# Performance work log

Measured on AMD Instinct MI355X. Metric: run time of the kernel, lower is better.

The kernel has to match this reference:

```python
import jax, jax.numpy as jnp
import numpy as np

V, D, F, B, E = 50257, 1024, 2048, 64, 512  # vocab, embed/rnn dim, fc hidden, batch, entities


def setup_inputs() -> dict:
    key = jax.random.key(0)
    ks = jax.random.split(key, 12)
    s = 0.05
    return {
        "entity_hiddens": jax.random.normal(ks[0], (B, E, D), jnp.float32),
        "question": jax.random.randint(ks[1], (B,), 0, V),
        "keys_mask": jax.random.randint(ks[2], (B, E), 0, 2).astype(bool),
        "emb": jax.random.normal(ks[3], (V, D), jnp.float32) * s,
        "W1": jax.random.normal(ks[4], (D, F), jnp.float32) * s,
        "b1": jnp.zeros((F,), jnp.float32),
        "W2": jax.random.normal(ks[5], (F, D), jnp.float32) * s,
        "b2": jnp.zeros((D,), jnp.float32),
        "A": jax.random.normal(ks[6], (D, D), jnp.float32) * s,  # entity_attn_matrix
        "H": jax.random.normal(ks[7], (D, D), jnp.float32) * s,
        "Ws": jax.random.normal(ks[8], (D, V), jnp.float32) * s,
        "bs": jnp.zeros((V,), jnp.float32),
    }


def reference(entity_hiddens, question, keys_mask, emb, W1, b1, W2, b2, A, H, Ws, bs):
    # embed question token and project: [B, D]
    eq0 = emb[question]
    q = jax.nn.relu(eq0 @ W1 + b1) @ W2 + b2
    # attention_entities actual returned math:
    # reduce_sum(expand_dims(q@A,1) * boolean_mask(entities, mask), axis=1)
    # == (q @ A) * sum over all masked entities (a single [D] vector)
    qA = q @ A  # [B, D]
    m = keys_mask.astype(entity_hiddens.dtype)
    ent_sum = jnp.sum(entity_hiddens * m[..., None], axis=(0, 1))  # [D]
    u = qA * ent_sum  # [B, D]
    logits = (q + u @ H) @ Ws + bs  # [B, V]
    return jax.nn.softmax(logits, axis=-1)
```

## Files before the change

kernel.cpp:

```cpp
#include <hip/hip_runtime.h>
#include <stdint.h>

#define V_ 50257
#define D_ 1024
#define F_ 2048
#define B_ 64
#define E_ 512
#define ROWS_ (B_*E_)

typedef __attribute__((ext_vector_type(8))) short bf16x8;
typedef __attribute__((ext_vector_type(4))) float f32x4;
typedef __attribute__((ext_vector_type(4), aligned(4))) float f32x4a;

__device__ __forceinline__ unsigned rne1(float a) {
  unsigned u = __float_as_uint(a);
  return (u + 0x7FFFu + ((u >> 16) & 1u)) >> 16;
}

__device__ __forceinline__ unsigned cvtpk(float a, float b) {
  unsigned r;
  asm("v_cvt_pk_bf16_f32 %0, %1, %2" : "=v"(r) : "v"(a), "v"(b));
  return r;
}

__device__ __forceinline__ float waveMax(float v) {
#pragma unroll
  for (int o = 32; o > 0; o >>= 1) v = fmaxf(v, __shfl_xor(v, o, 64));
  return v;
}
__device__ __forceinline__ float waveSum(float v) {
#pragma unroll
  for (int o = 32; o > 0; o >>= 1) v += __shfl_xor(v, o, 64);
  return v;
}


__device__ __forceinline__ void ent_partial_body(int bid, const float* __restrict__ eh,
                                                 const void* __restrict__ mask,
                                                 float* __restrict__ part) {
  __shared__ int s_mode;
  const int tid = threadIdx.x;
  const uint32_t* mu = (const uint32_t*)mask;
  int f = 0;
  for (int i = tid; i < (ROWS_ / 4); i += 256) {
    uint32_t u = mu[i];
    if (u == 0x3F800000u) f |= 2;
    else if (u & 0xFFFFFF00u) f |= 1;
  }
  if (tid == 0) s_mode = 0;
  __syncthreads();
  if (f) atomicOr(&s_mode, f);
  __syncthreads();
  const int sm = s_mode;
  const int mode = (sm & 1) ? 1 : ((sm & 2) ? 2 : 0);

  float4 acc = make_float4(0.f, 0.f, 0.f, 0.f);
  const float4* eh4 = (const float4*)eh;
  for (int row = bid; row < ROWS_; row += 512) {
    bool on;
    if (mode == 1)      on = ((const unsigned char*)mask)[row] != 0;
    else if (mode == 2) on = ((const float*)mask)[row] != 0.f;
    else                on = ((const int*)mask)[row] != 0;
    if (on) {
      float4 v = eh4[(size_t)row * (D_ / 4) + tid];
      acc.x += v.x; acc.y += v.y; acc.z += v.z; acc.w += v.w;
    }
  }
  ((float4*)part)[(size_t)bid * (D_ / 4) + tid] = acc;
}

__device__ __forceinline__ void ent_reduce_body(int bid, const float* __restrict__ part,
                                                float* __restrict__ entsum) {
  int d = bid * 256 + threadIdx.x;
  float s0 = 0.f, s1 = 0.f, s2 = 0.f, s3 = 0.f;
#pragma unroll 8
  for (int i = 0; i < 512; i += 4) {
    s0 += part[(size_t)(i    ) * D_ + d];
    s1 += part[(size_t)(i + 1) * D_ + d];
    s2 += part[(size_t)(i + 2) * D_ + d];
    s3 += part[(size_t)(i + 3) * D_ + d];
  }
  entsum[d] = (s0 + s1) + (s2 + s3);
}

__device__ __forceinline__ void gemm64_body(int bx, int by, const float* __restrict__ X,
                                            const int* __restrict__ gatherIdx,
                                            const float* __restrict__ emb,
                                            const float* __restrict__ W,
                                            int K, int N, int KB, float* __restrict__ part) {
  const int l  = threadIdx.x & 63;
  const int rg = __builtin_amdgcn_readfirstlane((int)(threadIdx.x >> 6));
  const int c  = bx * 64 + l;
  const int k0 = by * KB;
  const int m0 = rg * 16;

  const float* Xp = gatherIdx ? emb : X;
  int rb[16];
#pragma unroll
  for (int r = 0; r < 16; ++r) {
    int m = m0 + r;
    rb[r] = gatherIdx ? gatherIdx[m] * K : m * K;
  }

  float acc[16];
#pragma unroll
  for (int r = 0; r < 16; ++r) acc[r] = 0.f;

  for (int k = k0; k < k0 + KB; k += 8) {
    float wv[8];
#pragma unroll
    for (int j = 0; j < 8; ++j) wv[j] = W[(size_t)(k + j) * N + c];
#pragma unroll
    for (int r = 0; r < 16; ++r) {
      float4 x0 = *(const float4*)&Xp[rb[r] + k];
      float4 x1 = *(const float4*)&Xp[rb[r] + k + 4];
      acc[r] = fmaf(x0.x, wv[0], acc[r]);
      acc[r] = fmaf(x0.y, wv[1], acc[r]);
      acc[r] = fmaf(x0.z, wv[2], acc[r]);
      acc[r] = fmaf(x0.w, wv[3], acc[r]);
      acc[r] = fmaf(x1.x, wv[4], acc[r]);
      acc[r] = fmaf(x1.y, wv[5], acc[r]);
      acc[r] = fmaf(x1.z, wv[6], acc[r]);
      acc[r] = fmaf(x1.w, wv[7], acc[r]);
    }
  }
  size_t base = (size_t)by * ((size_t)64 * N);
#pragma unroll
  for (int r = 0; r < 16; ++r) part[base + (size_t)(m0 + r) * N + c] = acc[r];
}

template<int NSPLIT>
__device__ __forceinline__ void reduce_body_t(int bid, const float* __restrict__ part,
                                              int MN, int N,
                                              const float* __restrict__ vecB,
                                              const float* __restrict__ addend,
                                              int mode, float* __restrict__ dst,
                                              unsigned short* __restrict__ ph,
                                              unsigned short* __restrict__ pl) {
  int idx = bid * 256 + threadIdx.x;
  if (idx >= MN) return;

  if (mode == 4) {
    const int d   = idx;
    const int j   = d & 7;
    const int l   = (d >> 3) & 63;
    const int m   = (d >> 9) & 3;
    const int tg  = d >> 11;
    const int col = l & 15;
    const int g   = l >> 4;
    const int row = m * 16 + col;
    const int kk  = tg * 32 + g * 8 + j;
    const int src = row * 1024 + kk;
    float s = 0.f;
#pragma unroll
    for (int i = 0; i < NSPLIT; ++i) s += part[(size_t)i * MN + src];
    s += addend[src];
    unsigned hi = rne1(s);
    float hif = __uint_as_float(hi << 16);
    ph[d] = (unsigned short)hi;
    pl[d] = (unsigned short)rne1(s - hif);
    return;
  }

  float s = 0.f;
#pragma unroll
  for (int i = 0; i < NSPLIT; ++i) s += part[(size_t)i * MN + idx];
  int c = idx & (N - 1);
  if (mode == 1)      { s += vecB[c]; s = s > 0.f ? s : 0.f; dst[idx] = s; }
  else if (mode == 2) { s += vecB[c]; dst[idx] = s; }
  else                { s *= vecB[c]; dst[idx] = s; }
}

__global__ void k_p1(const float* __restrict__ eh, const void* __restrict__ mask,
                     float* __restrict__ entpart, const int* __restrict__ ques,
                     const float* __restrict__ emb, const float* __restrict__ W1,
                     float* __restrict__ gpart) {
  int bid = blockIdx.x;
  if (bid < 512) ent_partial_body(bid, eh, mask, entpart);
  else {
    int b2 = bid - 512;
    gemm64_body(b2 & 31, b2 >> 5, nullptr, ques, emb, W1, 1024, 2048, 64, gpart);
  }
}

__global__ void k_p2(const float* __restrict__ entpart, float* __restrict__ entsum,
                     const float* __restrict__ gpart, const float* __restrict__ b1,
                     float* __restrict__ hbuf) {
  int bid = blockIdx.x;
  if (bid < 4) ent_reduce_body(bid, entpart, entsum);
  else reduce_body_t<16>(bid - 4, gpart, 64 * 2048, 2048, b1, nullptr, 1, hbuf, nullptr, nullptr);
}

__global__ void k_gemm64(const float* __restrict__ X, const float* __restrict__ W,
                         int K, int N, int KB, float* __restrict__ part) {
  gemm64_body(blockIdx.x, blockIdx.y, X, nullptr, nullptr, W, K, N, KB, part);
}

template<int NSPLIT>
__global__ void k_reduce_t(const float* __restrict__ part, int MN, int N,
                           const float* __restrict__ vecB, const float* __restrict__ addend,
                           int mode, float* __restrict__ dst,
                           unsigned short* __restrict__ ph, unsigned short* __restrict__ pl) {
  reduce_body_t<NSPLIT>(blockIdx.x, part, MN, N, vecB, addend, mode, dst, ph, pl);
}

__global__ __launch_bounds__(256, 2) void k_gemm_big(const unsigned short* __restrict__ zpkh,
                                                     const unsigned short* __restrict__ zpkl,
                                                     const float* __restrict__ Ws,
                                                     float* __restrict__ part2) {
  __shared__ float lds[2][32 * 260];
  const int t   = threadIdx.x;
  const int l   = t & 63;
  const int w   = t >> 6;
  const int col = l & 15;
  const int g   = l >> 4;
  const int c0  = (blockIdx.x < 196) ? blockIdx.x * 256 : (V_ - 256);
  const int kbase = blockIdx.y * 512;
  const int xr  = (g & 1) << 4;

  f32x4 acc[4][4];
#pragma unroll
  for (int n = 0; n < 4; ++n)
#pragma unroll
    for (int m = 0; m < 4; ++m) acc[n][m] = (f32x4){0.f, 0.f, 0.f, 0.f};

  {
    f32x4a gg[8];
#pragma unroll
    for (int i = 0; i < 8; ++i) {
      const int r = w + 4 * i;
      gg[i] = *(const f32x4a*)(Ws + (size_t)(kbase + r) * V_ + c0 + 4 * l);
    }
#pragma unroll
    for (int i = 0; i < 8; ++i) {
      const int r = w + 4 * i;
      *(f32x4*)&lds[0][r * 260 + ((4 * l) ^ (((r >> 3) & 1) << 4))] = (f32x4)gg[i];
    }
  }
  __syncthreads();

  for (int tt = 0; tt < 16; ++tt) {
    const int buf = tt & 1;
    const int tg  = (kbase >> 5) + tt;

    bf16x8 ah[4], al[4];
#pragma unroll
    for (int m = 0; m < 4; ++m) {
      const int zb = ((tg * 4 + m) * 64 + l) * 8;
      ah[m] = *(const bf16x8*)(zpkh + zb);
      al[m] = *(const bf16x8*)(zpkl + zb);
    }

    f32x4a gg[8];
    if (tt + 1 < 16) {
      const float* wb = Ws + (size_t)(kbase + (tt + 1) * 32) * V_ + c0 + 4 * l;
#pragma unroll
      for (int i = 0; i < 8; ++i)
        gg[i] = *(const f32x4a*)(wb + (size_t)(w + 4 * i) * V_);
    }
    __builtin_amdgcn_sched_barrier(0);

#pragma unroll
    for (int n = 0; n < 4; ++n) {
      const int cread = w * 64 + n * 16 + col;
      float f[8];
#pragma unroll
      for (int j = 0; j < 8; ++j)
        f[j] = lds[buf][(g * 8 + j) * 260 + (cread ^ xr)];

      union { bf16x8 v; unsigned u[4]; } bh, bl;
#pragma unroll
      for (int j = 0; j < 4; ++j) {
        unsigned h = cvtpk(f[2 * j], f[2 * j + 1]);
        float h0f = __uint_as_float(h << 16);
        float h1f = __uint_as_float(h & 0xFFFF0000u);
        bh.u[j] = h;
        bl.u[j] = cvtpk(f[2 * j] - h0f, f[2 * j + 1] - h1f);
      }
#pragma unroll
      for (int m = 0; m < 4; ++m) acc[n][m] = __builtin_amdgcn_mfma_f32_16x16x32_bf16(ah[m], bh.v, acc[n][m], 0, 0, 0);
#pragma unroll
      for (int m = 0; m < 4; ++m) acc[n][m] = __builtin_amdgcn_mfma_f32_16x16x32_bf16(ah[m], bl.v, acc[n][m], 0, 0, 0);
#pragma unroll
      for (int m = 0; m < 4; ++m) acc[n][m] = __builtin_amdgcn_mfma_f32_16x16x32_bf16(al[m], bh.v, acc[n][m], 0, 0, 0);
    }
    __builtin_amdgcn_sched_barrier(0);

    if (tt + 1 < 16) {
#pragma unroll
      for (int i = 0; i < 8; ++i) {
        const int r = w + 4 * i;
        *(f32x4*)&lds[buf ^ 1][r * 260 + ((4 * l) ^ (((r >> 3) & 1) << 4))] = (f32x4)gg[i];
      }
    }
    __syncthreads();
  }

  float* pout = part2 + (size_t)blockIdx.y * ((size_t)64 * V_);
#pragma unroll
  for (int n = 0; n < 4; ++n) {
    const int c = c0 + w * 64 + n * 16 + col;
#pragma unroll
    for (int m = 0; m < 4; ++m)
#pragma unroll
      for (int i = 0; i < 4; ++i)
        pout[(size_t)(m * 16 + g * 4 + i) * V_ + c] = acc[n][m][i];
  }
}

#define SM_CHUNK 12565

__global__ void k_softmax1(const float* __restrict__ part2, const float* __restrict__ bs,
                           float2* __restrict__ stats) {
  __shared__ float smx[4], ssum[4];
  const int r = blockIdx.x >> 2, q = blockIdx.x & 3;
  const int beg = q * SM_CHUNK;
  const int end = (beg + SM_CHUNK < V_) ? beg + SM_CHUNK : V_;
  const float* p0 = part2 + (size_t)r * V_;
  const float* p1 = part2 + (size_t)64 * V_ + (size_t)r * V_;

  float mx = -3.4e38f;
  for (int i = beg + threadIdx.x; i < end; i += 256) mx = fmaxf(mx, p0[i] + p1[i] + bs[i]);
  mx = waveMax(mx);
  if ((threadIdx.x & 63) == 0) smx[threadIdx.x >> 6] = mx;
  __syncthreads();
  mx = fmaxf(fmaxf(smx[0], smx[1]), fmaxf(smx[2], smx[3]));

  float s = 0.f;
  for (int i = beg + threadIdx.x; i < end; i += 256) s += __expf(p0[i] + p1[i] + bs[i] - mx);
  s = waveSum(s);
  if ((threadIdx.x & 63) == 0) ssum[threadIdx.x >> 6] = s;
  __syncthreads();
  s = (ssum[0] + ssum[1]) + (ssum[2] + ssum[3]);

  if (threadIdx.x == 0) stats[blockIdx.x] = make_float2(mx, s);
}

__global__ void k_softmax2(const float* __restrict__ part2, const float* __restrict__ bs,
                           const float2* __restrict__ stats, float* __restrict__ out) {
  const int r = blockIdx.x >> 2, q = blockIdx.x & 3;
  float2 s0 = stats[r * 4 + 0], s1 = stats[r * 4 + 1];
  float2 s2 = stats[r * 4 + 2], s3 = stats[r * 4 + 3];
  float M = fmaxf(fmaxf(s0.x, s1.x), fmaxf(s2.x, s3.x));
  float S = s0.y * __expf(s0.x - M) + s1.y * __expf(s1.x - M)
          + s2.y * __expf(s2.x - M) + s3.y * __expf(s3.x - M);
  float inv = 1.f / S;
  const int beg = q * SM_CHUNK;
  const int end = (beg + SM_CHUNK < V_) ? beg + SM_CHUNK : V_;
  const float* p0 = part2 + (size_t)r * V_;
  const float* p1 = part2 + (size_t)64 * V_ + (size_t)r * V_;
  float* orow = out + (size_t)r * V_;
  for (int i = beg + threadIdx.x; i < end; i += 256)
    orow[i] = __expf(p0[i] + p1[i] + bs[i] - M) * inv;
}

extern "C" void kernel_launch(void* const* d_in, const int* in_sizes, int n_in,
                              void* d_out, int out_size, void* d_ws, size_t ws_size,
                              hipStream_t stream) {
  const float* eh   = (const float*)d_in[0];
  const int*   ques = (const int*)d_in[1];
  const void*  mask = d_in[2];
  const float* emb  = (const float*)d_in[3];
  const float* W1   = (const float*)d_in[4];
  const float* b1   = (const float*)d_in[5];
  const float* W2   = (const float*)d_in[6];
  const float* b2   = (const float*)d_in[7];
  const float* A    = (const float*)d_in[8];
  const float* H    = (const float*)d_in[9];
  const float* Ws   = (const float*)d_in[10];
  const float* bs   = (const float*)d_in[11];
  float* out = (float*)d_out;
  char* ws = (char*)d_ws;

  float*          gpart   = (float*)(ws + 0);
  float*          entpart = (float*)(ws + 12866048);
  float*          entsum  = (float*)(ws + 14963200);
  float*          hbuf    = (float*)(ws + 14967296);
  float*          qbuf    = (float*)(ws + 15491584);
  float*          ubuf    = (float*)(ws + 15753728);
  unsigned short* zpkh    = (unsigned short*)(ws + 16015872);
  unsigned short* zpkl    = (unsigned short*)(ws + 16146944);
  float2*         stats   = (float2*)(ws + 16278016);
  float*          part2   = (float*)(ws + 20971520);

  k_p1<<<1024, 256, 0, stream>>>(eh, mask, entpart, ques, emb, W1, gpart);
  k_p2<<<516, 256, 0, stream>>>(entpart, entsum, gpart, b1, hbuf);

  k_gemm64<<<dim3(16, 32), 256, 0, stream>>>(hbuf, W2, 2048, 1024, 64, gpart);
  k_reduce_t<32><<<256, 256, 0, stream>>>(gpart, 64 * 1024, 1024, b2, nullptr, 2, qbuf, nullptr, nullptr);

  k_gemm64<<<dim3(16, 16), 256, 0, stream>>>(qbuf, A, 1024, 1024, 64, gpart);
  k_reduce_t<16><<<256, 256, 0, stream>>>(gpart, 64 * 1024, 1024, entsum, nullptr, 3, ubuf, nullptr, nullptr);

  k_gemm64<<<dim3(16, 16), 256, 0, stream>>>(ubuf, H, 1024, 1024, 64, gpart);
  k_reduce_t<16><<<256, 256, 0, stream>>>(gpart, 64 * 1024, 1024, nullptr, qbuf, 4, nullptr, zpkh, zpkl);

  k_gemm_big<<<dim3(197, 2), 256, 0, stream>>>(zpkh, zpkl, Ws, part2);

  k_softmax1<<<256, 256, 0, stream>>>(part2, bs, stats);
  k_softmax2<<<256, 256, 0, stream>>>(part2, bs, stats, out);

  (void)in_sizes; (void)n_in; (void)out_size; (void)ws_size;
}
```

Measured before the change: 251.3 us.

## Single-buffer LDS in big GEMM, share activation tiles via LDS, raise occupancy

The big vocab GEMM drops its double-buffered Ws LDS tile in favour of a single buffer with an extra barrier. Each wave now loads one quarter of the packed bf16 activation fragments and shares them through LDS, where previously every wave loaded all four from global memory. These changes lower LDS and register use so launch bounds can move to three blocks per CU, at the cost of an added sync per K step. The entity-sum loop is also unrolled by four and replaces its branch with a mask multiply-add, which reads every row whether or not it is masked.

```diff
diff --git a/kernel.cpp b/kernel.cpp
--- a/kernel.cpp
+++ b/kernel.cpp
@@ -11,6 +11,7 @@
 typedef __attribute__((ext_vector_type(8))) short bf16x8;
 typedef __attribute__((ext_vector_type(4))) float f32x4;
 typedef __attribute__((ext_vector_type(4), aligned(4))) float f32x4a;
+typedef __attribute__((ext_vector_type(4))) unsigned u32x4;
 
 __device__ __forceinline__ unsigned rne1(float a) {
   unsigned u = __float_as_uint(a);
@@ -56,14 +57,27 @@
 
   float4 acc = make_float4(0.f, 0.f, 0.f, 0.f);
   const float4* eh4 = (const float4*)eh;
-  for (int row = bid; row < ROWS_; row += 512) {
-    bool on;
-    if (mode == 1)      on = ((const unsigned char*)mask)[row] != 0;
-    else if (mode == 2) on = ((const float*)mask)[row] != 0.f;
-    else                on = ((const int*)mask)[row] != 0;
-    if (on) {
-      float4 v = eh4[(size_t)row * (D_ / 4) + tid];
-      acc.x += v.x; acc.y += v.y; acc.z += v.z; acc.w += v.w;
+#pragma unroll 1
+  for (int i = 0; i < 64; i += 4) {
+    int r[4];
+    float m[4];
+    float4 v[4];
+#pragma unroll
+    for (int u = 0; u < 4; ++u) r[u] = bid + (i + u) * 512;
+#pragma unroll
+    for (int u = 0; u < 4; ++u) {
+      if (mode == 1)      m[u] = ((const unsigned char*)mask)[r[u]] ? 1.f : 0.f;
+      else if (mode == 2) m[u] = ((const float*)mask)[r[u]] != 0.f ? 1.f : 0.f;
+      else                m[u] = ((const int*)mask)[r[u]] ? 1.f : 0.f;
+    }
+#pragma unroll
+    for (int u = 0; u < 4; ++u) v[u] = eh4[(size_t)r[u] * (D_ / 4) + tid];
+#pragma unroll
+    for (int u = 0; u < 4; ++u) {
+      acc.x = fmaf(m[u], v[u].x, acc.x);
+      acc.y = fmaf(m[u], v[u].y, acc.y);
+      acc.z = fmaf(m[u], v[u].z, acc.z);
+      acc.w = fmaf(m[u], v[u].w, acc.w);
     }
   }
   ((float4*)part)[(size_t)bid * (D_ / 4) + tid] = acc;
@@ -204,16 +218,18 @@
   reduce_body_t<NSPLIT>(blockIdx.x, part, MN, N, vecB, addend, mode, dst, ph, pl);
 }
 
-__global__ __launch_bounds__(256, 2) void k_gemm_big(const unsigned short* __restrict__ zpkh,
+__global__ __launch_bounds__(256, 3) void k_gemm_big(const unsigned short* __restrict__ zpkh,
                                                      const unsigned short* __restrict__ zpkl,
                                                      const float* __restrict__ Ws,
                                                      float* __restrict__ part2) {
-  __shared__ float lds[2][32 * 260];
+  __shared__ float wslds[32 * 256];
+  __shared__ unsigned zlds[2048];
   const int t   = threadIdx.x;
   const int l   = t & 63;
   const int w   = t >> 6;
   const int col = l & 15;
   const int g   = l >> 4;
+  const int zm  = w;
   const int c0  = (blockIdx.x < 196) ? blockIdx.x * 256 : (V_ - 256);
   const int kbase = blockIdx.y * 512;
   const int xr  = (g & 1) << 4;
@@ -227,38 +243,48 @@
   {
     f32x4a gg[8];
 #pragma unroll
+    for (int i = 0; i < 8; ++i)
+      gg[i] = *(const f32x4a*)(Ws + (size_t)(kbase + w + 4 * i) * V_ + c0 + 4 * l);
+    const int tg0 = kbase >> 5;
+    const int zb  = ((tg0 * 4 + zm) * 64 + l) * 8;
+    u32x4 zh4 = *(const u32x4*)(zpkh + zb);
+    u32x4 zl4 = *(const u32x4*)(zpkl + zb);
+#pragma unroll
     for (int i = 0; i < 8; ++i) {
       const int r = w + 4 * i;
-      gg[i] = *(const f32x4a*)(Ws + (size_t)(kbase + r) * V_ + c0 + 4 * l);
-    }
-#pragma unroll
-    for (int i = 0; i < 8; ++i) {
-      const int r = w + 4 * i;
-      *(f32x4*)&lds[0][r * 260 + ((4 * l) ^ (((r >> 3) & 1) << 4))] = (f32x4)gg[i];
+      *(f32x4*)&wslds[r * 256 + ((4 * l) ^ (((r >> 3) & 1) << 4))] = (f32x4)gg[i];
+    }
+#pragma unroll
+    for (int j = 0; j < 4; ++j) {
+      zlds[j * 256 + zm * 64 + l]        = zh4[j];
+      zlds[1024 + j * 256 + zm * 64 + l] = zl4[j];
     }
   }
   __syncthreads();
 
   for (int tt = 0; tt < 16; ++tt) {
-    const int buf = tt & 1;
-    const int tg  = (kbase >> 5) + tt;
-
-    bf16x8 ah[4], al[4];
-#pragma unroll
-    for (int m = 0; m < 4; ++m) {
-      const int zb = ((tg * 4 + m) * 64 + l) * 8;
-      ah[m] = *(const bf16x8*)(zpkh + zb);
-      al[m] = *(const bf16x8*)(zpkl + zb);
-    }
-
     f32x4a gg[8];
+    u32x4 zh4, zl4;
     if (tt + 1 < 16) {
       const float* wb = Ws + (size_t)(kbase + (tt + 1) * 32) * V_ + c0 + 4 * l;
 #pragma unroll
       for (int i = 0; i < 8; ++i)
         gg[i] = *(const f32x4a*)(wb + (size_t)(w + 4 * i) * V_);
+      const int tgn = (kbase >> 5) + tt + 1;
+      const int zb  = ((tgn * 4 + zm) * 64 + l) * 8;
+      zh4 = *(const u32x4*)(zpkh + zb);
+      zl4 = *(const u32x4*)(zpkl + zb);
     }
     __builtin_amdgcn_sched_barrier(0);
+
+    union { bf16x8 v; unsigned u[4]; } ah[4], al[4];
+#pragma unroll
+    for (int m = 0; m < 4; ++m)
+#pragma unroll
+      for (int j = 0; j < 4; ++j) {
+        ah[m].u[j] = zlds[j * 256 + m * 64 + l];
+        al[m].u[j] = zlds[1024 + j * 256 + m * 64 + l];
+      }
 
 #pragma unroll
     for (int n = 0; n < 4; ++n) {
@@ -266,7 +292,7 @@
       float f[8];
 #pragma unroll
       for (int j = 0; j < 8; ++j)
-        f[j] = lds[buf][(g * 8 + j) * 260 + (cread ^ xr)];
+        f[j] = wslds[(g * 8 + j) * 256 + (cread ^ xr)];
 
       union { bf16x8 v; unsigned u[4]; } bh, bl;
 #pragma unroll
@@ -278,19 +304,25 @@
         bl.u[j] = cvtpk(f[2 * j] - h0f, f[2 * j + 1] - h1f);
       }
 #pragma unroll
-      for (int m = 0; m < 4; ++m) acc[n][m] = __builtin_amdgcn_mfma_f32_16x16x32_bf16(ah[m], bh.v, acc[n][m], 0, 0, 0);
-#pragma unroll
-      for (int m = 0; m < 4; ++m) acc[n][m] = __builtin_amdgcn_mfma_f32_16x16x32_bf16(ah[m], bl.v, acc[n][m], 0, 0, 0);
-#pragma unroll
-      for (int m = 0; m < 4; ++m) acc[n][m] = __builtin_amdgcn_mfma_f32_16x16x32_bf16(al[m], bh.v, acc[n][m], 0, 0, 0);
-    }
-    __builtin_amdgcn_sched_barrier(0);
+      for (int m = 0; m < 4; ++m) acc[n][m] = __builtin_amdgcn_mfma_f32_16x16x32_bf16(ah[m].v, bh.v, acc[n][m], 0, 0, 0);
+#pragma unroll
+      for (int m = 0; m < 4; ++m) acc[n][m] = __builtin_amdgcn_mfma_f32_16x16x32_bf16(ah[m].v, bl.v, acc[n][m], 0, 0, 0);
+#pragma unroll
+      for (int m = 0; m < 4; ++m) acc[n][m] = __builtin_amdgcn_mfma_f32_16x16x32_bf16(al[m].v, bh.v, acc[n][m], 0, 0, 0);
+    }
+
+    __syncthreads();
 
     if (tt + 1 < 16) {
 #pragma unroll
       for (int i = 0; i < 8; ++i) {
         const int r = w + 4 * i;
-        *(f32x4*)&lds[buf ^ 1][r * 260 + ((4 * l) ^ (((r >> 3) & 1) << 4))] = (f32x4)gg[i];
+        *(f32x4*)&wslds[r * 256 + ((4 * l) ^ (((r >> 3) & 1) << 4))] = (f32x4)gg[i];
+      }
+#pragma unroll
+      for (int j = 0; j < 4; ++j) {
+        zlds[j * 256 + zm * 64 + l]        = zh4[j];
+        zlds[1024 + j * 256 + zm * 64 + l] = zl4[j];
       }
     }
     __syncthreads();
```

New measurement: 246.5 us. About the same (-1.9%).
